# Kernel optimization log

Hardware: AMD Instinct MI355X
Metric: run time of the kernel (lower is better)

The kernel has to match this reference:

```python
import jax, jax.numpy as jnp
import numpy as np

B, T, C, H = 2, 2048, 768, 12
HD = C // H  # head dim = 64


def setup_inputs() -> dict:
    key = jax.random.key(0)
    k1, k2, k3 = jax.random.split(key, 3)
    s_in = 1.0 / np.sqrt(C)
    return {
        "x": jax.random.normal(k1, (B, T, C), dtype=jnp.float32),
        "Wqkv": jax.random.normal(k2, (C, 3 * C), dtype=jnp.float32) * s_in,
        "bqkv": jnp.zeros((3 * C,), dtype=jnp.float32),
        "Wproj": jax.random.normal(k3, (C, C), dtype=jnp.float32) * s_in,
        "bproj": jnp.zeros((C,), dtype=jnp.float32),
    }


def reference(x, Wqkv, bqkv, Wproj, bproj):
    b, t, c = x.shape
    qkv = x @ Wqkv + bqkv                      # [b, t, 3c]
    q, k, v = jnp.split(qkv, 3, axis=2)
    # [b, h, t, hd]
    q = q.reshape(b, t, H, HD).transpose(0, 2, 1, 3)
    k = k.reshape(b, t, H, HD).transpose(0, 2, 1, 3)
    v = v.reshape(b, t, H, HD).transpose(0, 2, 1, 3)
    scale = 1.0 / np.sqrt(HD)
    att = jnp.einsum("bhqd,bhkd->bhqk", q, k) * scale  # [b, h, t, t]
    causal = jnp.tril(jnp.ones((t, t), dtype=bool))
    att = jnp.where(causal[None, None], att, -jnp.inf)
    att = jax.nn.softmax(att, axis=-1)
    y = jnp.einsum("bhqk,bhkd->bhqd", att, v)          # [b, h, t, hd]
    y = y.transpose(0, 2, 1, 3).reshape(b, t, c)
    return y @ Wproj + bproj
```

## Files before the change

### kernel.cpp

```cpp
#include <hip/hip_runtime.h>
#include <math.h>

#define BB 2
#define TT 2048
#define CC 768
#define HH 12
#define HD 64
#define N3 (3*CC)

typedef __attribute__((ext_vector_type(8))) short short8;
typedef __attribute__((ext_vector_type(8))) _Float16 f16x8;
typedef __attribute__((ext_vector_type(4))) float f32x4;
typedef unsigned short u16;

#define QSCALE 0.1803368809f

static __device__ __forceinline__ u16 f2h(float x) {
    union { _Float16 h; u16 u; } v; v.h = (_Float16)x; return v.u;
}
static __device__ __forceinline__ float ex2(float x) {
#if __has_builtin(__builtin_amdgcn_exp2f)
    return __builtin_amdgcn_exp2f(x);
#else
    return exp2f(x);
#endif
}
static __device__ __forceinline__ unsigned pk2h(float a, float b) {
    auto p = __builtin_amdgcn_cvt_pkrtz(a, b);
    return __builtin_bit_cast(unsigned, p);
}

static __device__ __forceinline__ void gl16(const void* g, void* l) {
    __builtin_amdgcn_global_load_lds(
        (const __attribute__((address_space(1))) void*)g,
        (__attribute__((address_space(3))) void*)l, 16, 0, 0);
}

__global__ __launch_bounds__(256)
void conv_all(const float* __restrict__ x, u16* __restrict__ xh,
              const float* __restrict__ Wq, u16* __restrict__ wqh,
              const float* __restrict__ Wp, u16* __restrict__ wph)
{
    __shared__ float Tt[64][65];
    const int b = blockIdx.x;
    if (b < 3072) {
        const int i = b * 256 + threadIdx.x;
        float4 v = ((const float4*)x)[i];
        ushort4 o;
        o.x = f2h(v.x); o.y = f2h(v.y); o.z = f2h(v.z); o.w = f2h(v.w);
        ((ushort4*)xh)[i] = o;
        return;
    }
    const float* W; u16* T; int N, idx;
    if (b < 3504) { W = Wq; T = wqh; N = N3; idx = b - 3072; }
    else          { W = Wp; T = wph; N = CC; idx = b - 3504; }
    const int ntx = N / 64;
    const int n0 = (idx % ntx) * 64, k0 = (idx / ntx) * 64;
    const int tid = threadIdx.x;
    {
        const int r = tid >> 2, q = tid & 3;
        #pragma unroll
        for (int i = 0; i < 4; ++i) {
            float4 v = *(const float4*)(W + (size_t)(k0 + r) * N + n0 + q * 16 + i * 4);
            Tt[q * 16 + i * 4 + 0][r] = v.x;
            Tt[q * 16 + i * 4 + 1][r] = v.y;
            Tt[q * 16 + i * 4 + 2][r] = v.z;
            Tt[q * 16 + i * 4 + 3][r] = v.w;
        }
    }
    __syncthreads();
    {
        const int n = tid >> 2, q = tid & 3;
        u16 hh[16];
        #pragma unroll
        for (int j = 0; j < 16; ++j) hh[j] = f2h(Tt[n][q * 16 + j]);
        u16* dh = T + (size_t)(n0 + n) * 768 + k0 + q * 16;
        *(short8*)(dh) = *(short8*)&hh[0];
        *(short8*)(dh + 8) = *(short8*)&hh[8];
    }
}

template<int NCOLS, int MODE>
__global__ __launch_bounds__(256)
void mm3(const u16* __restrict__ A_g, const u16* __restrict__ B_g,
         const float* __restrict__ bias, float* __restrict__ outF,
         u16* __restrict__ qo, u16* __restrict__ ko, u16* __restrict__ vto)
{
    __shared__ u16 gsm[16384];
    char* smb = (char*)gsm;
    const int tid = threadIdx.x, lane = tid & 63, wv = tid >> 6;
    const int wm = wv >> 1, wn = wv & 1, r16 = lane & 15, kg = lane >> 4;
    const int m0 = blockIdx.y * 128, n0 = blockIdx.x * 128;

    const u16 *pA[2], *pB[2];
    int ldsq[2];
    #pragma unroll
    for (int qq = 0; qq < 2; ++qq) {
        const int L = wv * 2048 + qq * 1024 + lane * 16;
        const int row = L >> 6, c = (L >> 4) & 3;
        const int cp = c ^ ((row >> 1) & 3);
        ldsq[qq] = wv * 2048 + qq * 1024;
        pA[qq] = A_g + (size_t)(m0 + row) * 768 + cp * 8;
        pB[qq] = B_g + (size_t)(n0 + row) * 768 + cp * 8;
    }

    int aA[4], aB[4];
    #pragma unroll
    for (int t = 0; t < 4; ++t) {
        const int rA = wm * 64 + t * 16 + r16;
        const int rB = wn * 64 + t * 16 + r16;
        aA[t] = rA * 64 + ((kg ^ ((rA >> 1) & 3)) << 4);
        aB[t] = rB * 64 + ((kg ^ ((rB >> 1) & 3)) << 4) + 8192;
    }

    f32x4 acc[4][4];
    #pragma unroll
    for (int i = 0; i < 4; ++i)
        #pragma unroll
        for (int j = 0; j < 4; ++j) acc[i][j] = (f32x4)0.f;

    #pragma unroll
    for (int qq = 0; qq < 2; ++qq) {
        gl16(pA[qq], smb + ldsq[qq]);
        gl16(pB[qq], smb + 8192 + ldsq[qq]);
        pA[qq] += 32; pB[qq] += 32;
    }
    __syncthreads();

    int cur = 0;
    for (int ks = 0; ks < 24; ++ks) {
        const int nxt = cur ^ 1;
        if (ks != 23) {
            #pragma unroll
            for (int qq = 0; qq < 2; ++qq) {
                gl16(pA[qq], smb + nxt * 16384 + ldsq[qq]);
                gl16(pB[qq], smb + nxt * 16384 + 8192 + ldsq[qq]);
                pA[qq] += 32; pB[qq] += 32;
            }
        }
        const int cb = cur * 16384;
        f16x8 a[4], b[4];
        #pragma unroll
        for (int t = 0; t < 4; ++t) {
            a[t] = *(const f16x8*)(smb + cb + aA[t]);
            b[t] = *(const f16x8*)(smb + cb + aB[t]);
        }
        #pragma unroll
        for (int mt = 0; mt < 4; ++mt)
            #pragma unroll
            for (int nt = 0; nt < 4; ++nt)
                acc[mt][nt] = __builtin_amdgcn_mfma_f32_16x16x32_f16(a[mt], b[nt], acc[mt][nt], 0, 0, 0);
        __syncthreads();
        cur = nxt;
    }

    float bi[4];
    #pragma unroll
    for (int nt = 0; nt < 4; ++nt) bi[nt] = bias[n0 + wn * 64 + nt * 16 + r16];

    if (MODE == 1) {
        #pragma unroll
        for (int mt = 0; mt < 4; ++mt)
            #pragma unroll
            for (int nt = 0; nt < 4; ++nt)
                #pragma unroll
                for (int r = 0; r < 4; ++r) {
                    const int grow = m0 + wm * 64 + mt * 16 + kg * 4 + r;
                    const int gcol = n0 + wn * 64 + nt * 16 + r16;
                    outF[(size_t)grow * CC + gcol] = acc[mt][nt][r] + bi[nt];
                }
    } else {
        const int which = n0 / CC;
        const float qsc = (which == 0) ? QSCALE : 1.0f;
        const int b_ = m0 >> 11;
        #pragma unroll
        for (int mt = 0; mt < 4; ++mt) {
            const int tb = ((m0 & 2047) + wm * 64 + mt * 16 + kg * 4);
            #pragma unroll
            for (int nt = 0; nt < 4; ++nt) {
                const int gcol = n0 + wn * 64 + nt * 16 + r16;
                const int cc = gcol - which * CC;
                const int h = cc >> 6, d = cc & 63;
                const int bh_ = b_ * HH + h;
                if (which == 2) {
                    ushort4 hv;
                    #pragma unroll
                    for (int r = 0; r < 4; ++r)
                        ((u16*)&hv)[r] = f2h(acc[mt][nt][r] + bi[nt]);
                    *(ushort4*)(vto + ((size_t)bh_ * 64 + d) * 2048 + tb) = hv;
                } else {
                    u16* dst = (which == 0) ? qo : ko;
                    #pragma unroll
                    for (int r = 0; r < 4; ++r)
                        dst[(((size_t)bh_ * 2048 + tb + r) << 6) + d] =
                            f2h((acc[mt][nt][r] + bi[nt]) * qsc);
                }
            }
        }
    }
}

__global__ __launch_bounds__(64)
void attn3(const u16* __restrict__ qp, const u16* __restrict__ kp,
           const u16* __restrict__ vtp, u16* __restrict__ attp)
{
    __shared__ u16 smem[10240];
    char* smb = (char*)smem;

    const int lane = threadIdx.x;
    const int bid = blockIdx.x;
    const int qt = 63 - (bid / 24);
    const int bh = bid % 24;
    const int t0 = qt * 32;
    const int r16 = lane & 15, kg = lane >> 4;
    const int kg4 = kg * 4, kg8 = kg * 8;
    const int pwx = (r16 & 7) << 4;

    const size_t qroA = ((size_t)bh * TT + t0 + r16) * 64;
    f16x8 qfA[2], qfB[2];
    #pragma unroll
    for (int ks = 0; ks < 2; ++ks) {
        qfA[ks] = *(const f16x8*)(qp + qroA + ks * 32 + kg8);
        qfB[ks] = *(const f16x8*)(qp + qroA + 1024 + ks * 32 + kg8);
    }

    const u16 *pk[4], *pv[4];
    #pragma unroll
    for (int rr = 0; rr < 4; ++rr) {
        const int key0 = rr * 8 + (lane >> 3);
        const int cpk  = (lane & 7) ^ (lane >> 3);
        pk[rr] = kp + ((size_t)bh * TT + key0) * 64 + cpk * 8;
        const int d0  = rr * 16 + (lane >> 2);
        const int cpv = (lane & 3) ^ ((lane >> 2) & 3);
        pv[rr] = vtp + ((size_t)(bh * 64 + d0)) * TT + cpv * 8;
    }

    int aK[2][2], aV[4], aP[2], pw[2];
    #pragma unroll
    for (int ks = 0; ks < 2; ++ks)
        #pragma unroll
        for (int nt = 0; nt < 2; ++nt) {
            const int row = nt * 16 + r16;
            aK[ks][nt] = row * 128 + (((ks * 4 + kg) ^ (row & 7)) << 4);
        }
    #pragma unroll
    for (int nt = 0; nt < 4; ++nt) {
        const int d = nt * 16 + r16;
        aV[nt] = 4096 + d * 64 + ((kg ^ (d & 3)) << 4);
    }
    #pragma unroll
    for (int s = 0; s < 2; ++s) {
        aP[s] = 16384 + s * 2048 + r16 * 128 + ((kg ^ (r16 & 7)) << 4);
        pw[s] = 16384 + s * 2048 + r16 * 128;
    }

    f32x4 oA[4], oB[4];
    #pragma unroll
    for (int i = 0; i < 4; ++i) { oA[i] = (f32x4)0.f; oB[i] = (f32x4)0.f; }
    f32x4 lA = (f32x4)0.f, lB = (f32x4)0.f;
    float mA = -1e30f, mB = -1e30f;

    f16x8 ones;
    #pragma unroll
    for (int i = 0; i < 8; ++i) ones[i] = (_Float16)1.0f;

    auto stage = [&](int bufb) {
        #pragma unroll
        for (int rr = 0; rr < 4; ++rr) {
            gl16(pk[rr], smb + bufb + rr * 1024);
            gl16(pv[rr], smb + bufb + 4096 + rr * 1024);
            pk[rr] += 2048;
            pv[rr] += 32;
        }
    };

    stage(0);
    int cur = 0;
    for (int j = 0; j <= qt; ++j) {
        if (j < qt) {
            stage((cur ^ 1) * 8192);
            asm volatile("s_waitcnt vmcnt(8)" ::: "memory");
        } else {
            asm volatile("s_waitcnt vmcnt(0)" ::: "memory");
        }
        const int cb = cur * 8192;

        f32x4 sA[2], sB[2];
        sA[0] = (f32x4)0.f; sA[1] = (f32x4)0.f;
        sB[0] = (f32x4)0.f; sB[1] = (f32x4)0.f;
        __builtin_amdgcn_s_setprio(1);
        #pragma unroll
        for (int ks = 0; ks < 2; ++ks)
            #pragma unroll
            for (int nt = 0; nt < 2; ++nt) {
                f16x8 kf = *(const f16x8*)(smb + cb + aK[ks][nt]);
                sA[nt] = __builtin_amdgcn_mfma_f32_16x16x32_f16(kf, qfA[ks], sA[nt], 0, 0, 0);
                sB[nt] = __builtin_amdgcn_mfma_f32_16x16x32_f16(kf, qfB[ks], sB[nt], 0, 0, 0);
            }
        __builtin_amdgcn_s_setprio(0);

        if (j == qt) {
            #pragma unroll
            for (int nt = 0; nt < 2; ++nt)
                #pragma unroll
                for (int r = 0; r < 4; ++r) {
                    const int keyo = nt * 16 + kg4 + r;
                    if (keyo > r16)      sA[nt][r] = -1e30f;
                    if (keyo > 16 + r16) sB[nt][r] = -1e30f;
                }
        }

        auto softmax = [&](f32x4 (&s)[2], float& m, f32x4& ol, f32x4 (&oa)[4],
                           int pwb) {
            float pm = fmaxf(fmaxf(fmaxf(s[0][0], s[0][1]), fmaxf(s[0][2], s[0][3])),
                             fmaxf(fmaxf(s[1][0], s[1][1]), fmaxf(s[1][2], s[1][3])));
            pm = fmaxf(pm, __shfl_xor(pm, 16));
            pm = fmaxf(pm, __shfl_xor(pm, 32));
            if (__any(pm > m + 8.0f)) {
                const float mn = fmaxf(m, pm);
                const float corr = ex2(m - mn);
                m = mn;
                const float c0 = __shfl(corr, kg4 + 0);
                const float c1 = __shfl(corr, kg4 + 1);
                const float c2 = __shfl(corr, kg4 + 2);
                const float c3 = __shfl(corr, kg4 + 3);
                #pragma unroll
                for (int nt = 0; nt < 4; ++nt) {
                    oa[nt][0] *= c0; oa[nt][1] *= c1;
                    oa[nt][2] *= c2; oa[nt][3] *= c3;
                }
                ol[0] *= c0; ol[1] *= c1; ol[2] *= c2; ol[3] *= c3;
            }
            #pragma unroll
            for (int nt = 0; nt < 2; ++nt) {
                uint2 w;
                w.x = pk2h(ex2(s[nt][0] - m), ex2(s[nt][1] - m));
                w.y = pk2h(ex2(s[nt][2] - m), ex2(s[nt][3] - m));
                *(uint2*)(smb + pwb + ((nt * 32 + kg8) ^ pwx)) = w;
            }
        };
        softmax(sA, mA, lA, oA, pw[0]);
        softmax(sB, mB, lB, oB, pw[1]);

        __builtin_amdgcn_s_setprio(1);
        f16x8 paA = *(const f16x8*)(smb + aP[0]);
        f16x8 paB = *(const f16x8*)(smb + aP[1]);
        lA = __builtin_amdgcn_mfma_f32_16x16x32_f16(paA, ones, lA, 0, 0, 0);
        lB = __builtin_amdgcn_mfma_f32_16x16x32_f16(paB, ones, lB, 0, 0, 0);
        #pragma unroll
        for (int nt = 0; nt < 4; ++nt) {
            f16x8 vf = *(const f16x8*)(smb + cb + aV[nt]);
            oA[nt] = __builtin_amdgcn_mfma_f32_16x16x32_f16(paA, vf, oA[nt], 0, 0, 0);
            oB[nt] = __builtin_amdgcn_mfma_f32_16x16x32_f16(paB, vf, oB[nt], 0, 0, 0);
        }
        __builtin_amdgcn_s_setprio(0);

        cur ^= 1;
    }

    const int b_ = bh / HH, h = bh % HH;
    #pragma unroll
    for (int r = 0; r < 4; ++r) {
        const float invA = 1.f / lA[r];
        const float invB = 1.f / lB[r];
        const int tA = t0 + kg4 + r;
        const size_t baseA = ((size_t)b_ * TT + tA) * CC + h * 64;
        const size_t baseB = baseA + (size_t)16 * CC;
        #pragma unroll
        for (int nt = 0; nt < 4; ++nt) {
            attp[baseA + nt * 16 + r16] = f2h(oA[nt][r] * invA);
            attp[baseB + nt * 16 + r16] = f2h(oB[nt][r] * invB);
        }
    }
}

extern "C" void kernel_launch(void* const* d_in, const int* in_sizes, int n_in,
                              void* d_out, int out_size, void* d_ws, size_t ws_size,
                              hipStream_t stream)
{
    const float* x     = (const float*)d_in[0];
    const float* Wqkv  = (const float*)d_in[1];
    const float* bqkv  = (const float*)d_in[2];
    const float* Wproj = (const float*)d_in[3];
    const float* bproj = (const float*)d_in[4];
    float* out = (float*)d_out;

    const size_t E  = (size_t)4096 * 768;
    const size_t WQ = (size_t)2304 * 768;
    const size_t WP = (size_t)768 * 768;

    u16* ws   = (u16*)d_ws;
    u16* xh   = ws;
    u16* atth = ws;
    u16* wqh  = ws + E;
    u16* wph  = wqh + WQ;
    u16* qh   = wph + WP;
    u16* kh   = qh + E;
    u16* vth  = kh + E;

    conv_all<<<dim3(3648), 256, 0, stream>>>(x, xh, Wqkv, wqh, Wproj, wph);

    mm3<N3, 0><<<dim3(N3 / 128, 32), 256, 0, stream>>>(
        xh, wqh, bqkv, nullptr, qh, kh, vth);
    attn3<<<dim3(1536), 64, 0, stream>>>(qh, kh, vth, atth);
    mm3<CC, 1><<<dim3(CC / 128, 32), 256, 0, stream>>>(
        atth, wph, bproj, out, nullptr, nullptr, nullptr);
}
```

Measured before the change: 179.6 us.

## Split causal attention over KV chunks and add a combine kernel

Each query tile's key range is split into slices of up to 16 key tiles, so the attention launch grows from 1536 to 3840 one-wave blocks with more even per-block work. Each block writes a partial output in fp16 plus its row max and sum, and a new combine kernel merges the slices with log-sum-exp rescaling. This is meant to cut the long tail from the causal imbalance, where late query tiles loop over many more key tiles than early ones. The cost is an extra launch, extra global traffic for the partials, and an extra fp16 rounding step. The V-tile LDS swizzle is also changed along with the slicing.

```diff
diff --git a/kernel.cpp b/kernel.cpp
--- a/kernel.cpp
+++ b/kernel.cpp
@@ -17,6 +17,9 @@
 
 static __device__ __forceinline__ u16 f2h(float x) {
     union { _Float16 h; u16 u; } v; v.h = (_Float16)x; return v.u;
+}
+static __device__ __forceinline__ float h2f(u16 x) {
+    union { u16 u; _Float16 h; } v; v.u = x; return (float)v.h;
 }
 static __device__ __forceinline__ float ex2(float x) {
 #if __has_builtin(__builtin_amdgcn_exp2f)
@@ -202,16 +205,25 @@
 
 __global__ __launch_bounds__(64)
 void attn3(const u16* __restrict__ qp, const u16* __restrict__ kp,
-           const u16* __restrict__ vtp, u16* __restrict__ attp)
+           const u16* __restrict__ vtp, float* __restrict__ mpart,
+           float* __restrict__ lpart, u16* __restrict__ opart)
 {
     __shared__ u16 smem[10240];
     char* smb = (char*)smem;
 
     const int lane = threadIdx.x;
     const int bid = blockIdx.x;
-    const int qt = 63 - (bid / 24);
     const int bh = bid % 24;
+    const int g = bid / 24;
+    int qt, sl;
+    if (g < 16)      { qt = g;                              sl = 0;     }
+    else if (g < 48) { const int t = g - 16; qt = 16 + (t >> 1); sl = t & 1; }
+    else if (g < 96) { const int t = g - 48; qt = 32 + t / 3;    sl = t % 3; }
+    else             { const int t = g - 96; qt = 48 + (t >> 2); sl = t & 3; }
     const int t0 = qt * 32;
+    const int jstart = sl * 16;
+    const int jend = (jstart + 16 < qt + 1) ? (jstart + 16) : (qt + 1);
+
     const int r16 = lane & 15, kg = lane >> 4;
     const int kg4 = kg * 4, kg8 = kg * 8;
     const int pwx = (r16 & 7) << 4;
@@ -229,10 +241,10 @@
     for (int rr = 0; rr < 4; ++rr) {
         const int key0 = rr * 8 + (lane >> 3);
         const int cpk  = (lane & 7) ^ (lane >> 3);
-        pk[rr] = kp + ((size_t)bh * TT + key0) * 64 + cpk * 8;
+        pk[rr] = kp + ((size_t)bh * TT + jstart * 32 + key0) * 64 + cpk * 8;
         const int d0  = rr * 16 + (lane >> 2);
-        const int cpv = (lane & 3) ^ ((lane >> 2) & 3);
-        pv[rr] = vtp + ((size_t)(bh * 64 + d0)) * TT + cpv * 8;
+        const int cpv = (lane & 3) ^ ((lane >> 3) & 3);
+        pv[rr] = vtp + ((size_t)(bh * 64 + d0)) * TT + jstart * 32 + cpv * 8;
     }
 
     int aK[2][2], aV[4], aP[2], pw[2];
@@ -246,7 +258,7 @@
     #pragma unroll
     for (int nt = 0; nt < 4; ++nt) {
         const int d = nt * 16 + r16;
-        aV[nt] = 4096 + d * 64 + ((kg ^ (d & 3)) << 4);
+        aV[nt] = 4096 + d * 64 + ((kg ^ ((r16 >> 1) & 3)) << 4);
     }
     #pragma unroll
     for (int s = 0; s < 2; ++s) {
@@ -259,6 +271,7 @@
     for (int i = 0; i < 4; ++i) { oA[i] = (f32x4)0.f; oB[i] = (f32x4)0.f; }
     f32x4 lA = (f32x4)0.f, lB = (f32x4)0.f;
     float mA = -1e30f, mB = -1e30f;
+    float mtA = -1e30f, mtB = -1e30f;
 
     f16x8 ones;
     #pragma unroll
@@ -276,8 +289,8 @@
 
     stage(0);
     int cur = 0;
-    for (int j = 0; j <= qt; ++j) {
-        if (j < qt) {
+    for (int j = jstart; j < jend; ++j) {
+        if (j + 1 < jend) {
             stage((cur ^ 1) * 8192);
             asm volatile("s_waitcnt vmcnt(8)" ::: "memory");
         } else {
@@ -310,12 +323,13 @@
                 }
         }
 
-        auto softmax = [&](f32x4 (&s)[2], float& m, f32x4& ol, f32x4 (&oa)[4],
-                           int pwb) {
+        auto softmax = [&](f32x4 (&s)[2], float& m, float& mt, f32x4& ol,
+                           f32x4 (&oa)[4], int pwb) {
             float pm = fmaxf(fmaxf(fmaxf(s[0][0], s[0][1]), fmaxf(s[0][2], s[0][3])),
                              fmaxf(fmaxf(s[1][0], s[1][1]), fmaxf(s[1][2], s[1][3])));
             pm = fmaxf(pm, __shfl_xor(pm, 16));
             pm = fmaxf(pm, __shfl_xor(pm, 32));
+            mt = fmaxf(mt, pm);
             if (__any(pm > m + 8.0f)) {
                 const float mn = fmaxf(m, pm);
                 const float corr = ex2(m - mn);
@@ -339,8 +353,8 @@
                 *(uint2*)(smb + pwb + ((nt * 32 + kg8) ^ pwx)) = w;
             }
         };
-        softmax(sA, mA, lA, oA, pw[0]);
-        softmax(sB, mB, lB, oB, pw[1]);
+        softmax(sA, mA, mtA, lA, oA, pw[0]);
+        softmax(sB, mB, mtB, lB, oB, pw[1]);
 
         __builtin_amdgcn_s_setprio(1);
         f16x8 paA = *(const f16x8*)(smb + aP[0]);
@@ -358,20 +372,85 @@
         cur ^= 1;
     }
 
+    const float fA = ex2(mA - mtA);
+    const float fB = ex2(mB - mtB);
+    float cA[4], cB[4], mAr[4], mBr[4];
+    #pragma unroll
+    for (int r = 0; r < 4; ++r) {
+        cA[r] = __shfl(fA, kg4 + r);
+        cB[r] = __shfl(fB, kg4 + r);
+        mAr[r] = __shfl(mtA, kg4 + r);
+        mBr[r] = __shfl(mtB, kg4 + r);
+    }
+    #pragma unroll
+    for (int nt = 0; nt < 4; ++nt)
+        #pragma unroll
+        for (int r = 0; r < 4; ++r) {
+            oA[nt][r] *= cA[r];
+            oB[nt][r] *= cB[r];
+        }
+    #pragma unroll
+    for (int r = 0; r < 4; ++r) { lA[r] *= cA[r]; lB[r] *= cB[r]; }
+
+    const size_t pbase = (size_t)(sl * 24 + bh) * 2048;
+    #pragma unroll
+    for (int r = 0; r < 4; ++r) {
+        const int rowA = t0 + kg4 + r;
+        const int rowB = rowA + 16;
+        #pragma unroll
+        for (int nt = 0; nt < 4; ++nt) {
+            opart[(pbase + rowA) * 64 + nt * 16 + r16] = f2h(oA[nt][r]);
+            opart[(pbase + rowB) * 64 + nt * 16 + r16] = f2h(oB[nt][r]);
+        }
+        if (r16 == 0) {
+            mpart[pbase + rowA] = mAr[r];
+            mpart[pbase + rowB] = mBr[r];
+            lpart[pbase + rowA] = lA[r];
+            lpart[pbase + rowB] = lB[r];
+        }
+    }
+}
+
+__global__ __launch_bounds__(256)
+void attn_comb(const float* __restrict__ mpart, const float* __restrict__ lpart,
+               const u16* __restrict__ opart, u16* __restrict__ attp)
+{
+    const int blk = blockIdx.x;
+    const int bh = blk >> 6;
+    const int row = ((blk & 63) << 5) + (threadIdx.x >> 3);
+    const int dc = (threadIdx.x & 7) * 8;
+    const int nsl = (row >> 9) + 1;
+
+    float mv[4], lv[4];
+    float M = -1e30f;
+    #pragma unroll
+    for (int s = 0; s < 4; ++s)
+        if (s < nsl) {
+            mv[s] = mpart[(size_t)(s * 24 + bh) * 2048 + row];
+            lv[s] = lpart[(size_t)(s * 24 + bh) * 2048 + row];
+            M = fmaxf(M, mv[s]);
+        }
+    float L = 0.f;
+    float acc[8];
+    #pragma unroll
+    for (int i = 0; i < 8; ++i) acc[i] = 0.f;
+    #pragma unroll
+    for (int s = 0; s < 4; ++s)
+        if (s < nsl) {
+            const float w = ex2(mv[s] - M);
+            L += w * lv[s];
+            short8 o8 = *(const short8*)(opart +
+                ((size_t)(s * 24 + bh) * 2048 + row) * 64 + dc);
+            #pragma unroll
+            for (int i = 0; i < 8; ++i)
+                acc[i] += w * h2f((u16)o8[i]);
+        }
+    const float inv = 1.f / L;
     const int b_ = bh / HH, h = bh % HH;
-    #pragma unroll
-    for (int r = 0; r < 4; ++r) {
-        const float invA = 1.f / lA[r];
-        const float invB = 1.f / lB[r];
-        const int tA = t0 + kg4 + r;
-        const size_t baseA = ((size_t)b_ * TT + tA) * CC + h * 64;
-        const size_t baseB = baseA + (size_t)16 * CC;
-        #pragma unroll
-        for (int nt = 0; nt < 4; ++nt) {
-            attp[baseA + nt * 16 + r16] = f2h(oA[nt][r] * invA);
-            attp[baseB + nt * 16 + r16] = f2h(oB[nt][r] * invB);
-        }
-    }
+    u16 o[8];
+    #pragma unroll
+    for (int i = 0; i < 8; ++i) o[i] = f2h(acc[i] * inv);
+    *(short8*)(attp + ((size_t)b_ * TT + row) * CC + h * 64 + dc) = *(short8*)o;
 }
 
 extern "C" void kernel_launch(void* const* d_in, const int* in_sizes, int n_in,
@@ -388,6 +467,7 @@
     const size_t E  = (size_t)4096 * 768;
     const size_t WQ = (size_t)2304 * 768;
     const size_t WP = (size_t)768 * 768;
+    const size_t PR = (size_t)4 * 24 * 2048;
 
     u16* ws   = (u16*)d_ws;
     u16* xh   = ws;
@@ -397,12 +477,16 @@
     u16* qh   = wph + WP;
     u16* kh   = qh + E;
     u16* vth  = kh + E;
+    float* mpart = (float*)(vth + E);
+    float* lpart = mpart + PR;
+    u16*   opart = (u16*)(lpart + PR);
 
     conv_all<<<dim3(3648), 256, 0, stream>>>(x, xh, Wqkv, wqh, Wproj, wph);
 
     mm3<N3, 0><<<dim3(N3 / 128, 32), 256, 0, stream>>>(
         xh, wqh, bqkv, nullptr, qh, kh, vth);
-    attn3<<<dim3(1536), 64, 0, stream>>>(qh, kh, vth, atth);
+    attn3<<<dim3(3840), 64, 0, stream>>>(qh, kh, vth, mpart, lpart, opart);
+    attn_comb<<<dim3(1536), 256, 0, stream>>>(mpart, lpart, opart, atth);
     mm3<CC, 1><<<dim3(CC / 128, 32), 256, 0, stream>>>(
         atth, wph, bproj, out, nullptr, nullptr, nullptr);
 }
```

After: 168.4 us. 1.07x faster.
